# Optimization experiments

Hardware: AMD Instinct MI355X
Metric: run time of the kernel (lower is better)

The kernel has to match this reference:

```python
import jax, jax.numpy as jnp
import numpy as np

N = 20000      # num nodes
E = 320000     # num edges
F_IN = 512
HEADS = 8
D = 64         # out_features per head (512 / 8)
ALPHA = 0.2    # leaky relu slope
EPS = 1e-16


def setup_inputs() -> dict:
    key = jax.random.key(0)
    k1, k2, k3, k4, k5 = jax.random.split(key, 5)
    x = jax.random.normal(k1, (N, F_IN), dtype=jnp.float32)
    edge_index = jax.random.randint(k2, (2, E), 0, N, dtype=jnp.int64)
    # per-head parameters (xavier-normal-ish scale)
    s_w = np.sqrt(2.0 / (F_IN + D))
    W_e = jax.random.normal(k3, (HEADS, F_IN, D), dtype=jnp.float32) * s_w
    W_r = jax.random.normal(k4, (HEADS, F_IN, D), dtype=jnp.float32) * s_w
    # attention vector over concat of [h_src, h_dst, diff, |diff|, prod] -> 5*D
    s_a = np.sqrt(2.0 / (1 + 5 * D))
    a = jax.random.normal(k5, (HEADS, 5 * D), dtype=jnp.float32) * s_a
    return {"x": x, "edge_index": edge_index, "W_e": W_e, "W_r": W_r, "a": a}


def _gat_forward(x, edge_index, W_e, W_r, a):
    src = edge_index[0]  # [E] softmax / output rows
    dst = edge_index[1]  # [E]

    h_e = jnp.einsum('nf,hfd->hnd', x, W_e)  # [H,N,D]
    h_r = jnp.einsum('nf,hfd->hnd', x, W_r)  # [H,N,D]

    a_src, a_dst, a_dif, a_abs, a_prd = jnp.split(a, 5, axis=1)  # each [H,D]

    # node-level dot products for the linear concat parts, then gather
    s_src = jnp.einsum('hnd,hd->hn', h_e, a_src)[:, src]  # [H,E]
    s_dst = jnp.einsum('hnd,hd->hn', h_e, a_dst)[:, dst]  # [H,E]

    hr_src = h_r[:, src]            # [H,E,D]
    hr_dst = h_r[:, dst]            # [H,E,D]
    diff = hr_dst - hr_src          # [H,E,D]
    score = (s_src + s_dst
             + jnp.einsum('hed,hd->he', diff, a_dif)
             + jnp.einsum('hed,hd->he', jnp.abs(diff), a_abs)
             + jnp.einsum('hed,hd->he', hr_src * hr_dst, a_prd))  # [H,E]

    alpha = jax.nn.leaky_relu(score, negative_slope=ALPHA)  # [H,E]

    # sparse softmax over edges grouped by source node
    alpha_t = alpha.T  # [E,H]
    m = jax.ops.segment_max(alpha_t, src, num_segments=N)        # [N,H]
    ex = jnp.exp(alpha_t - m[src])                                # [E,H]
    denom = jax.ops.segment_sum(ex, src, num_segments=N)[src]    # [E,H]
    att = ex / (denom + EPS)                                      # [E,H]

    # spmm: out[src] += att * h_e[dst]
    msg = att[:, :, None] * jnp.transpose(h_e[:, dst], (1, 0, 2))  # [E,H,D]
    out = jax.ops.segment_sum(msg, src, num_segments=N)            # [N,H,D]
    return out.reshape(N, HEADS * D)  # concat heads along feature dim


def reference(x, edge_index, W_e, W_r, a):
    return _gat_forward(x, edge_index, W_e, W_r, a)
```

## Files before the change

kernel.cpp:

```cpp
#include <hip/hip_runtime.h>
#include <hip/hip_bf16.h>

#define N_NODES 20000
#define N_EDGES 320000
#define F_IN 512
#define HEADS 8
#define DH 64
#define KPAD 64

typedef _Float16 f16;
typedef __attribute__((ext_vector_type(8))) _Float16 half8;
typedef __attribute__((ext_vector_type(4))) _Float16 half4v;
typedef __attribute__((ext_vector_type(2))) _Float16 half2v;
typedef __attribute__((ext_vector_type(4))) float f32x4;

__device__ __forceinline__ void async_copy16(void* lds_base, const void* g) {
  __builtin_amdgcn_global_load_lds(
      (const __attribute__((address_space(1))) unsigned int*)g,
      (__attribute__((address_space(3))) unsigned int*)lds_base, 16, 0, 0);
}

#define CX_BLOCKS 2500
#define CW_BLOCKS 128
#define WA_BLOCKS 16

__global__ __launch_bounds__(256) void prologue_kernel(
    const float* __restrict__ x, const float* __restrict__ We,
    const float* __restrict__ Wr, const float* __restrict__ a,
    f16* __restrict__ xh, f16* __restrict__ Wt)
{
  __shared__ f16 tile[64 * 65];
  const int b = blockIdx.x;
  if (b < CX_BLOCKS) {
    int base = (b * 256 + threadIdx.x) * 4;
    #pragma unroll
    for (int rep = 0; rep < 4; ++rep) {
      int i = base + rep * (CX_BLOCKS * 256 * 4);
      float4 v = *(const float4*)&x[i];
      half4v o;
      o[0] = (f16)v.x; o[1] = (f16)v.y; o[2] = (f16)v.z; o[3] = (f16)v.w;
      *(half4v*)&xh[i] = o;
    }
  } else if (b < CX_BLOCKS + CW_BLOCKS) {
    const int bb = b - CX_BLOCKS;
    const int kt = (bb & 7) * 64;
    const int h = (bb >> 3) & 7;
    const int mat = bb >> 6;
    const float* __restrict__ W = (mat ? Wr : We) + (size_t)h * F_IN * DH;
    #pragma unroll
    for (int r = 0; r < 16; ++r) {
      int idx = r * 256 + threadIdx.x;
      int k = idx >> 6, d = idx & 63;
      tile[d * 65 + k] = (f16)W[(size_t)(kt + k) * DH + d];
    }
    __syncthreads();
    f16* __restrict__ Wo = Wt + (size_t)(mat * 8 + h) * 64 * F_IN;
    #pragma unroll
    for (int r = 0; r < 16; ++r) {
      int idx = r * 256 + threadIdx.x;
      int d = idx >> 6, k = idx & 63;
      Wo[(size_t)d * F_IN + kt + k] = tile[d * 65 + k];
    }
  } else {
    const int j = b - CX_BLOCKS - CW_BLOCKS;
    const int h = j & 7, sel = j >> 3;
    const float* __restrict__ ae = a + h * 320 + (sel ? 64 : 0);
    const float* __restrict__ ad = a + h * 320 + 128;
    const float sgn = sel ? 1.f : -1.f;
    #pragma unroll
    for (int rep = 0; rep < 2; ++rep) {
      int k = rep * 256 + threadIdx.x;
      const float* __restrict__ we = We + ((size_t)h * F_IN + k) * DH;
      const float* __restrict__ wr = Wr + ((size_t)h * F_IN + k) * DH;
      float s = 0.f;
      #pragma unroll
      for (int d = 0; d < DH; ++d)
        s = fmaf(we[d], ae[d], fmaf(sgn * wr[d], ad[d], s));
      Wt[(size_t)(1024 + j) * F_IN + k] = (f16)s;
    }
  }
}

#define GBM 128
#define GBN 128
#define GBK 64
#define MT_TOTAL 157
#define MT_PER_GRP 20
#define NCT 9
#define NKT (F_IN / GBK)
#define TSTR 72
#define GEMM_GRID (8 * MT_PER_GRP * NCT)
#define SCAT_BLOCKS 1250

__global__ __launch_bounds__(256) void gemm_mfma(
    const f16* __restrict__ xh, const f16* __restrict__ Wt,
    f16* __restrict__ hef,
    float* __restrict__ ssrc, float* __restrict__ sdst,
    const int* __restrict__ ei, int* __restrict__ cnt, int* __restrict__ csr)
{
  const int b = blockIdx.x;
  if (b >= GEMM_GRID) {
    int e = (b - GEMM_GRID) * 256 + threadIdx.x;
    if (e < N_EDGES) {
      int s = ei[e];
      int t = ei[N_EDGES + e];
      int pos = atomicAdd(&cnt[s], 1);
      if (pos < KPAD) csr[s * KPAD + pos] = t;
    }
    return;
  }

  const int g = b & 7;
  const int j = b >> 3;
  const int mg = j / NCT;
  const int m_tile = g * MT_PER_GRP + mg;
  const int c_tile = j - mg * NCT;
  if (m_tile >= MT_TOTAL) return;

  __shared__ f16 smem[32768];
  f16* __restrict__ As = smem;
  f16* __restrict__ Bs = smem + 16384;
  const int tid = threadIdx.x;
  const int m0 = m_tile * GBM;
  const int n0 = c_tile * GBN;
  const int wv = tid >> 6, lane = tid & 63, quad = lane >> 4, l16 = lane & 15;
  const int wm = (wv >> 1) * 64;
  const int wn = (wv & 1) * 64;
  const int lrow = lane >> 3;
  const int gc = (lane & 7) ^ (lrow & 7);

  f32x4 acc[4][4] = {};

  auto stage = [&](int kt, int buf) {
    #pragma unroll
    for (int s = 0; s < 4; ++s) {
      int seg = wv * 4 + s;
      int row = seg * 8 + lrow;
      async_copy16(&As[buf * 8192 + seg * 512],
                   &xh[(size_t)(m0 + row) * F_IN + kt + gc * 8]);
      async_copy16(&Bs[buf * 8192 + seg * 512],
                   &Wt[(size_t)(n0 + row) * F_IN + kt + gc * 8]);
    }
  };

  stage(0, 0);
  __syncthreads();
  for (int it = 0; it < NKT; ++it) {
    if (it + 1 < NKT) stage((it + 1) * GBK, (it + 1) & 1);
    const f16* __restrict__ Ab = &As[(it & 1) * 8192];
    const f16* __restrict__ Bb = &Bs[(it & 1) * 8192];
    #pragma unroll
    for (int ks = 0; ks < 2; ++ks) {
      half8 af[4], bf4[4];
      const int ch = ((ks << 2) + quad) ^ (l16 & 7);
      #pragma unroll
      for (int i = 0; i < 4; ++i)
        af[i] = *(const half8*)&Ab[(wm + i * 16 + l16) * GBK + ch * 8];
      #pragma unroll
      for (int jj = 0; jj < 4; ++jj)
        bf4[jj] = *(const half8*)&Bb[(wn + jj * 16 + l16) * GBK + ch * 8];
      #pragma unroll
      for (int i = 0; i < 4; ++i)
        #pragma unroll
        for (int jj = 0; jj < 4; ++jj)
          acc[i][jj] = __builtin_amdgcn_mfma_f32_16x16x32_f16(af[i], bf4[jj], acc[i][jj], 0, 0, 0);
    }
    __syncthreads();
  }

  const int cb = c_tile * 2 + (wv & 1);
  const int mat = cb >> 3, h = cb & 7;

  if (mat < 2) {
    f16* __restrict__ tb = smem + wv * (64 * TSTR);
    #pragma unroll
    for (int i = 0; i < 4; ++i)
      #pragma unroll
      for (int jj = 0; jj < 4; ++jj)
        #pragma unroll
        for (int r = 0; r < 4; ++r)
          tb[(i * 16 + quad * 4 + r) * TSTR + jj * 16 + l16] = (f16)acc[i][jj][r];
    const int rrow = lane >> 3;
    const int rseg = lane & 7;
    #pragma unroll
    for (int g2 = 0; g2 < 8; ++g2) {
      int row = g2 * 8 + rrow;
      half8 vv = *(const half8*)&tb[row * TSTR + rseg * 8];
      int m = m0 + wm + row;
      if (m < N_NODES)
        *(half8*)&hef[(size_t)m * 1024 + mat * 512 + h * DH + rseg * 8] = vv;
    }
  } else if (cb == 16) {
    #pragma unroll
    for (int i = 0; i < 4; ++i) {
      #pragma unroll
      for (int r = 0; r < 4; ++r) {
        int m = m0 + wm + i * 16 + quad * 4 + r;
        if (m < N_NODES) {
          float v = acc[i][0][r];
          if (l16 < 8) ssrc[(size_t)m * HEADS + l16] = v;
          else         sdst[(size_t)m * HEADS + (l16 - 8)] = v;
        }
      }
    }
  }
}

__global__ __launch_bounds__(256) void attn_kernel(
    const f16* __restrict__ hef, const float* __restrict__ a,
    const float* __restrict__ ssrc, const float* __restrict__ sdst,
    const int* __restrict__ cnt, const int* __restrict__ csr,
    float* __restrict__ out)
{
  const int wv = threadIdx.x >> 6;
  const int n = blockIdx.x * 4 + wv;
  const int lane = threadIdx.x & 63;
  const int h = lane >> 3;
  const int d0 = (lane & 7) * 8;
  const int deg = min(cnt[n], KPAD);
  const int beg = n * KPAD, end = beg + deg;

  const half8 hrn = *(const half8*)&hef[(size_t)n * 1024 + lane * 8 + 512];
  half2v aabs2[4], aprd2[4];
  const int ab = h * 320;
  #pragma unroll
  for (int c = 0; c < 4; ++c) {
    aabs2[c][0] = (f16)a[ab + 192 + d0 + 2 * c];
    aabs2[c][1] = (f16)a[ab + 192 + d0 + 2 * c + 1];
    aprd2[c][0] = (f16)a[ab + 256 + d0 + 2 * c];
    aprd2[c][1] = (f16)a[ab + 256 + d0 + 2 * c + 1];
  }
  const float sbase = ssrc[(size_t)n * HEADS + h];

  float denom = 0.f;
  float acc[8] = {};

  auto edge = [&](half8 he8, half8 hr8, float sd) {
    half8 df = hr8 - hrn;
    uint4 u = __builtin_bit_cast(uint4, df);
    u.x &= 0x7FFF7FFFu; u.y &= 0x7FFF7FFFu; u.z &= 0x7FFF7FFFu; u.w &= 0x7FFF7FFFu;
    half8 ad = __builtin_bit_cast(half8, u);
    half8 pr = hr8 * hrn;
    float va = 0.f, vb = 0.f;
    #pragma unroll
    for (int c = 0; c < 4; ++c) {
      half2v ad2 = {ad[2 * c], ad[2 * c + 1]};
      half2v pr2 = {pr[2 * c], pr[2 * c + 1]};
      va = __builtin_amdgcn_fdot2(ad2, aabs2[c], va, false);
      vb = __builtin_amdgcn_fdot2(pr2, aprd2[c], vb, false);
    }
    float v = va + vb;
    v += __shfl_xor(v, 1);
    v += __shfl_xor(v, 2);
    v += __shfl_xor(v, 4);
    float sc = sbase + sd + v;
    sc = fmaxf(sc, 0.2f * sc);
    float ex = __expf(sc);
    denom += ex;
    #pragma unroll
    for (int jj = 0; jj < 8; ++jj) acc[jj] = fmaf(ex, (float)he8[jj], acc[jj]);
  };

  int i = beg;
  for (; i + 2 <= end; i += 2) {
    int t0 = csr[i], t1 = csr[i + 1];
    size_t b0 = (size_t)t0 * 1024 + lane * 8;
    size_t b1 = (size_t)t1 * 1024 + lane * 8;
    half8 e0 = *(const half8*)&hef[b0];
    half8 r0 = *(const half8*)&hef[b0 + 512];
    half8 e1 = *(const half8*)&hef[b1];
    half8 r1 = *(const half8*)&hef[b1 + 512];
    float s0 = sdst[(size_t)t0 * HEADS + h];
    float s1 = sdst[(size_t)t1 * HEADS + h];
    edge(e0, r0, s0);
    edge(e1, r1, s1);
  }
  if (i < end) {
    int t = csr[i];
    size_t b0 = (size_t)t * 1024 + lane * 8;
    half8 e0 = *(const half8*)&hef[b0];
    half8 r0 = *(const half8*)&hef[b0 + 512];
    edge(e0, r0, sdst[(size_t)t * HEADS + h]);
  }

  float inv = 1.f / (denom + 1e-16f);
  float4 o0, o1;
  o0.x = acc[0] * inv; o0.y = acc[1] * inv; o0.z = acc[2] * inv; o0.w = acc[3] * inv;
  o1.x = acc[4] * inv; o1.y = acc[5] * inv; o1.z = acc[6] * inv; o1.w = acc[7] * inv;
  *(float4*)&out[(size_t)n * 512 + lane * 8] = o0;
  *(float4*)&out[(size_t)n * 512 + lane * 8 + 4] = o1;
}

extern "C" void kernel_launch(void* const* d_in, const int* in_sizes, int n_in,
                              void* d_out, int out_size, void* d_ws, size_t ws_size,
                              hipStream_t stream) {
  const float* x  = (const float*)d_in[0];
  const int*   ei = (const int*)d_in[1];
  const float* We = (const float*)d_in[2];
  const float* Wr = (const float*)d_in[3];
  const float* a  = (const float*)d_in[4];
  float* out = (float*)d_out;

  char* ws = (char*)d_ws;
  size_t p = 0;
  auto alloc = [&](size_t bytes) {
    void* r = ws + p;
    p = (p + bytes + 255) & ~(size_t)255;
    return r;
  };
  f16* xh  = (f16*)alloc(sizeof(f16) * (size_t)N_NODES * F_IN);
  f16* Wt  = (f16*)alloc(sizeof(f16) * (size_t)1152 * F_IN);
  f16* hef = (f16*)alloc(sizeof(f16) * (size_t)N_NODES * 1024);
  float* ssrc = (float*)alloc(sizeof(float) * (size_t)N_NODES * HEADS);
  float* sdst = (float*)alloc(sizeof(float) * (size_t)N_NODES * HEADS);
  int* cnt = (int*)alloc(sizeof(int) * N_NODES);
  int* csr = (int*)alloc(sizeof(int) * (size_t)N_NODES * KPAD);

  hipMemsetAsync(cnt, 0, sizeof(int) * N_NODES, stream);

  prologue_kernel<<<CX_BLOCKS + CW_BLOCKS + WA_BLOCKS, 256, 0, stream>>>(
      x, We, Wr, a, xh, Wt);

  gemm_mfma<<<GEMM_GRID + SCAT_BLOCKS, 256, 0, stream>>>(
      xh, Wt, hef, ssrc, sdst, ei, cnt, csr);

  attn_kernel<<<N_NODES / 4, 256, 0, stream>>>(hef, a, ssrc, sdst, cnt, csr, out);
}
```

Baseline: 235.4 us.

## Use 8-wave GEMM blocks with 64x32 warp tiles and fold counter zeroing into prologue

```diff
diff --git a/kernel.cpp b/kernel.cpp
--- a/kernel.cpp
+++ b/kernel.cpp
@@ -27,10 +27,17 @@
 __global__ __launch_bounds__(256) void prologue_kernel(
     const float* __restrict__ x, const float* __restrict__ We,
     const float* __restrict__ Wr, const float* __restrict__ a,
-    f16* __restrict__ xh, f16* __restrict__ Wt)
+    f16* __restrict__ xh, f16* __restrict__ Wt, int* __restrict__ cnt)
 {
   __shared__ f16 tile[64 * 65];
   const int b = blockIdx.x;
+  if (b < 20) {
+    int idx = b * 256 + threadIdx.x;
+    if (idx < 5000) {
+      int4 z; z.x = 0; z.y = 0; z.z = 0; z.w = 0;
+      ((int4*)cnt)[idx] = z;
+    }
+  }
   if (b < CX_BLOCKS) {
     int base = (b * 256 + threadIdx.x) * 4;
     #pragma unroll
@@ -88,11 +95,11 @@
 #define MT_PER_GRP 20
 #define NCT 9
 #define NKT (F_IN / GBK)
-#define TSTR 72
+#define TSTR2 40
 #define GEMM_GRID (8 * MT_PER_GRP * NCT)
-#define SCAT_BLOCKS 1250
-
-__global__ __launch_bounds__(256) void gemm_mfma(
+#define SCAT_BLOCKS 625
+
+__global__ __launch_bounds__(512) void gemm_mfma(
     const f16* __restrict__ xh, const f16* __restrict__ Wt,
     f16* __restrict__ hef,
     float* __restrict__ ssrc, float* __restrict__ sdst,
@@ -100,7 +107,7 @@
 {
   const int b = blockIdx.x;
   if (b >= GEMM_GRID) {
-    int e = (b - GEMM_GRID) * 256 + threadIdx.x;
+    int e = (b - GEMM_GRID) * 512 + threadIdx.x;
     if (e < N_EDGES) {
       int s = ei[e];
       int t = ei[N_EDGES + e];
@@ -124,17 +131,17 @@
   const int m0 = m_tile * GBM;
   const int n0 = c_tile * GBN;
   const int wv = tid >> 6, lane = tid & 63, quad = lane >> 4, l16 = lane & 15;
-  const int wm = (wv >> 1) * 64;
-  const int wn = (wv & 1) * 64;
+  const int wm = (wv >> 2) * 64;
+  const int wn = (wv & 3) * 32;
   const int lrow = lane >> 3;
   const int gc = (lane & 7) ^ (lrow & 7);
 
-  f32x4 acc[4][4] = {};
+  f32x4 acc[4][2] = {};
 
   auto stage = [&](int kt, int buf) {
     #pragma unroll
-    for (int s = 0; s < 4; ++s) {
-      int seg = wv * 4 + s;
+    for (int s = 0; s < 2; ++s) {
+      int seg = wv * 2 + s;
       int row = seg * 8 + lrow;
       async_copy16(&As[buf * 8192 + seg * 512],
                    &xh[(size_t)(m0 + row) * F_IN + kt + gc * 8]);
@@ -151,46 +158,50 @@
     const f16* __restrict__ Bb = &Bs[(it & 1) * 8192];
     #pragma unroll
     for (int ks = 0; ks < 2; ++ks) {
-      half8 af[4], bf4[4];
+      half8 af[4], bf2[2];
       const int ch = ((ks << 2) + quad) ^ (l16 & 7);
       #pragma unroll
       for (int i = 0; i < 4; ++i)
         af[i] = *(const half8*)&Ab[(wm + i * 16 + l16) * GBK + ch * 8];
       #pragma unroll
-      for (int jj = 0; jj < 4; ++jj)
-        bf4[jj] = *(const half8*)&Bb[(wn + jj * 16 + l16) * GBK + ch * 8];
+      for (int jj = 0; jj < 2; ++jj)
+        bf2[jj] = *(const half8*)&Bb[(wn + jj * 16 + l16) * GBK + ch * 8];
       #pragma unroll
       for (int i = 0; i < 4; ++i)
         #pragma unroll
-        for (int jj = 0; jj < 4; ++jj)
-          acc[i][jj] = __builtin_amdgcn_mfma_f32_16x16x32_f16(af[i], bf4[jj], acc[i][jj], 0, 0, 0);
+        for (int jj = 0; jj < 2; ++jj)
+          acc[i][jj] = __builtin_amdgcn_mfma_f32_16x16x32_f16(af[i], bf2[jj], acc[i][jj], 0, 0, 0);
     }
     __syncthreads();
   }
 
-  const int cb = c_tile * 2 + (wv & 1);
-  const int mat = cb >> 3, h = cb & 7;
-
-  if (mat < 2) {
-    f16* __restrict__ tb = smem + wv * (64 * TSTR);
+  const int cb32 = c_tile * 4 + (wv & 3);
+  const int col0 = cb32 * 32;
+
+  if (c_tile < 8) {
+    const int mat = col0 >> 9;
+    const int hcol = col0 & 511;
+    const int h = hcol >> 6;
+    const int hh = (hcol >> 5) & 1;
+    f16* __restrict__ tb = smem + wv * (64 * TSTR2);
     #pragma unroll
     for (int i = 0; i < 4; ++i)
       #pragma unroll
-      for (int jj = 0; jj < 4; ++jj)
+      for (int jj = 0; jj < 2; ++jj)
         #pragma unroll
         for (int r = 0; r < 4; ++r)
-          tb[(i * 16 + quad * 4 + r) * TSTR + jj * 16 + l16] = (f16)acc[i][jj][r];
-    const int rrow = lane >> 3;
-    const int rseg = lane & 7;
-    #pragma unroll
-    for (int g2 = 0; g2 < 8; ++g2) {
-      int row = g2 * 8 + rrow;
-      half8 vv = *(const half8*)&tb[row * TSTR + rseg * 8];
+          tb[(i * 16 + quad * 4 + r) * TSTR2 + jj * 16 + l16] = (f16)acc[i][jj][r];
+    const int rrow = lane >> 2;
+    const int rseg = lane & 3;
+    #pragma unroll
+    for (int g2 = 0; g2 < 4; ++g2) {
+      int row = g2 * 16 + rrow;
+      half8 vv = *(const half8*)&tb[row * TSTR2 + rseg * 8];
       int m = m0 + wm + row;
       if (m < N_NODES)
-        *(half8*)&hef[(size_t)m * 1024 + mat * 512 + h * DH + rseg * 8] = vv;
-    }
-  } else if (cb == 16) {
+        *(half8*)&hef[(size_t)m * 1024 + mat * 512 + h * DH + hh * 32 + rseg * 8] = vv;
+    }
+  } else if ((wv & 3) == 0) {
     #pragma unroll
     for (int i = 0; i < 4; ++i) {
       #pragma unroll
@@ -316,12 +327,10 @@
   int* cnt = (int*)alloc(sizeof(int) * N_NODES);
   int* csr = (int*)alloc(sizeof(int) * (size_t)N_NODES * KPAD);
 
-  hipMemsetAsync(cnt, 0, sizeof(int) * N_NODES, stream);
-
   prologue_kernel<<<CX_BLOCKS + CW_BLOCKS + WA_BLOCKS, 256, 0, stream>>>(
-      x, We, Wr, a, xh, Wt);
-
-  gemm_mfma<<<GEMM_GRID + SCAT_BLOCKS, 256, 0, stream>>>(
+      x, We, Wr, a, xh, Wt, cnt);
+
+  gemm_mfma<<<GEMM_GRID + SCAT_BLOCKS, 512, 0, stream>>>(
       xh, Wt, hef, ssrc, sdst, ei, cnt, csr);
 
   attn_kernel<<<N_NODES / 4, 256, 0, stream>>>(hef, a, ssrc, sdst, cnt, csr, out);
```

New measurement: 236.1 us. Within noise of the previous version (+0.3%).
